# Kernel optimization log

Hardware: AMD Instinct MI355X
Metric: run time of the kernel (lower is better)

Reference implementation:

```python
import jax, jax.numpy as jnp
import numpy as np
import math

B, S, T, F_IN, D = 4, 4096, 4096, 127, 64

def setup_inputs() -> dict:
    key = jax.random.key(0)
    k1, k2, k3, k4 = jax.random.split(key, 4)
    return {
        "x1": jax.random.normal(k1, (B, S, F_IN), dtype=jnp.float32),
        "x2": jax.random.normal(k2, (B, T, F_IN), dtype=jnp.float32),
        "W": jax.random.normal(k3, (D, F_IN), dtype=jnp.float32) * (1.0 / math.sqrt(F_IN)),
        "b": jax.random.normal(k4, (D,), dtype=jnp.float32) * 0.01,
    }

def reference(x1, x2, W, b):
    # shared linear projection: torch Linear -> x @ W.T + b
    q = jnp.einsum('bsf,df->bsd', x1, W) + b   # [B,S,D]
    k = jnp.einsum('btf,df->btd', x2, W) + b   # [B,T,D]
    scores = jnp.einsum('bsd,btd->bst', q, k)  # [B,S,T]
    # faithful to source: v4 = v3.div(1/sqrt(D)) == v3 * sqrt(D)
    scores = scores * jnp.sqrt(jnp.float32(D))
    p = jax.nn.softmax(scores, axis=-1)        # [B,S,T]
    # dropout p=0.01 treated as eval-mode identity (deterministic reference)
    out = jnp.einsum('bst,btf->bsf', p, x2)    # [B,S,F_IN]
    return out
```

## Files before the change

### kernel.cpp

```cpp
#include <hip/hip_runtime.h>
#include <hip/hip_bf16.h>


typedef __bf16 bf16x8 __attribute__((ext_vector_type(8)));
typedef float f32x16 __attribute__((ext_vector_type(16)));

#define S_DIM 4096
#define F_DIM 127
#define QSCALE 11.5415603271f
#define THR 11.0f

static __device__ __forceinline__ unsigned cvt_pk_bf16(float lo, float hi) {
  unsigned r;
  asm("v_cvt_pk_bf16_f32 %0, %1, %2" : "=v"(r) : "v"(lo), "v"(hi));
  return r;
}
static __device__ __forceinline__ float exp2_fast(float x) {
  float r;
  asm("v_exp_f32 %0, %1" : "=v"(r) : "v"(x));
  return r;
}
static __device__ __forceinline__ float m3(float a, float b, float c) {
  return fmaxf(fmaxf(a, b), c);
}
static __device__ __forceinline__ bf16x8 mk_bf16x8(unsigned w0, unsigned w1,
                                                   unsigned w2, unsigned w3) {
  unsigned t[4] = {w0, w1, w2, w3};
  bf16x8 r;
  __builtin_memcpy(&r, t, 16);
  return r;
}
static __device__ __forceinline__ bf16x8 u4_bf16x8(uint4 v) {
  bf16x8 r;
  __builtin_memcpy(&r, &v, 16);
  return r;
}
static __device__ __forceinline__ void split8(float4 a, float4 b, bf16x8& hv,
                                              bf16x8& lv) {
  const unsigned h0 = cvt_pk_bf16(a.x, a.y);
  const unsigned h1 = cvt_pk_bf16(a.z, a.w);
  const unsigned h2 = cvt_pk_bf16(b.x, b.y);
  const unsigned h3 = cvt_pk_bf16(b.z, b.w);
  const unsigned l0 = cvt_pk_bf16(a.x - __uint_as_float(h0 << 16),
                                  a.y - __uint_as_float(h0 & 0xffff0000u));
  const unsigned l1 = cvt_pk_bf16(a.z - __uint_as_float(h1 << 16),
                                  a.w - __uint_as_float(h1 & 0xffff0000u));
  const unsigned l2 = cvt_pk_bf16(b.x - __uint_as_float(h2 << 16),
                                  b.y - __uint_as_float(h2 & 0xffff0000u));
  const unsigned l3 = cvt_pk_bf16(b.z - __uint_as_float(h3 << 16),
                                  b.w - __uint_as_float(h3 & 0xffff0000u));
  hv = mk_bf16x8(h0, h1, h2, h3);
  lv = mk_bf16x8(l0, l1, l2, l3);
}

__global__ __launch_bounds__(256) void prep_kernel(
    const float* __restrict__ x1, const float* __restrict__ x2,
    const float* __restrict__ W, const float* __restrict__ bias,
    uint4* __restrict__ qhf, uint4* __restrict__ qlf,
    uint4* __restrict__ khf, uint4* __restrict__ klf,
    uint4* __restrict__ x2tf) {
  __shared__ unsigned shbuf[8448];
  const int tid = threadIdx.x;
  const int bi = blockIdx.x;

  if (bi >= 256) {
    const int ri = bi - 256;
    const int b = ri >> 8;
    const int tt = ri & 255;
    const int fb = tid >> 6;
    const int l = tid & 63;
    const int t0 = tt * 16 + ((l >> 5) << 3);
    const int f = fb * 32 + (l & 31);
    const float* src = x2 + ((long)b * S_DIM + t0) * F_DIM + f;
    unsigned w[4];
#pragma unroll
    for (int g = 0; g < 4; ++g) {
      const float v0 = (f < F_DIM) ? src[(long)(2 * g) * F_DIM] : 1.0f;
      const float v1 = (f < F_DIM) ? src[(long)(2 * g + 1) * F_DIM] : 1.0f;
      w[g] = cvt_pk_bf16(v0, v1);
    }
    x2tf[((long)(b * 256 + tt) * 4 + fb) * 64 + l] =
        make_uint4(w[0], w[1], w[2], w[3]);
    return;
  }

  float* shw = (float*)shbuf;
  for (int idx = tid; idx < 64 * 128; idx += 256) {
    const int d = idx >> 7;
    const int f = idx & 127;
    shw[d * 132 + f] = (f < F_DIM) ? W[d * F_DIM + f] : 0.f;
  }
  __syncthreads();

  const int wave = tid >> 6;
  const int lane = tid & 63;
  const int arow = lane & 31;
  const int half = lane >> 5;
  const bool isK = bi >= 128;
  const float* x = isK ? x2 : x1;
  const int grow0 = (bi & 127) * 128 + wave * 32;
  const float* xrow = x + (long)(grow0 + arow) * F_DIM;

  bf16x8 xh[8], xl[8];
#pragma unroll
  for (int kk = 0; kk < 8; ++kk) {
    const int f0 = kk * 16 + half * 8;
    float4 a, b;
    a.x = (f0 + 0 < F_DIM) ? xrow[f0 + 0] : 0.f;
    a.y = (f0 + 1 < F_DIM) ? xrow[f0 + 1] : 0.f;
    a.z = (f0 + 2 < F_DIM) ? xrow[f0 + 2] : 0.f;
    a.w = (f0 + 3 < F_DIM) ? xrow[f0 + 3] : 0.f;
    b.x = (f0 + 4 < F_DIM) ? xrow[f0 + 4] : 0.f;
    b.y = (f0 + 5 < F_DIM) ? xrow[f0 + 5] : 0.f;
    b.z = (f0 + 6 < F_DIM) ? xrow[f0 + 6] : 0.f;
    b.w = (f0 + 7 < F_DIM) ? xrow[f0 + 7] : 0.f;
    split8(a, b, xh[kk], xl[kk]);
  }

  f32x16 acc0, acc1;
#pragma unroll
  for (int r = 0; r < 16; ++r) {
    acc0[r] = 0.f;
    acc1[r] = 0.f;
  }
#pragma unroll
  for (int kk = 0; kk < 8; ++kk) {
    const int f0 = kk * 16 + half * 8;
    bf16x8 wh0, wl0, wh1, wl1;
    {
      const float4 a = *(const float4*)&shw[arow * 132 + f0];
      const float4 b = *(const float4*)&shw[arow * 132 + f0 + 4];
      split8(a, b, wh0, wl0);
    }
    {
      const float4 a = *(const float4*)&shw[(32 + arow) * 132 + f0];
      const float4 b = *(const float4*)&shw[(32 + arow) * 132 + f0 + 4];
      split8(a, b, wh1, wl1);
    }
    acc0 = __builtin_amdgcn_mfma_f32_32x32x16_bf16(xh[kk], wh0, acc0, 0, 0, 0);
    acc0 = __builtin_amdgcn_mfma_f32_32x32x16_bf16(xh[kk], wl0, acc0, 0, 0, 0);
    acc0 = __builtin_amdgcn_mfma_f32_32x32x16_bf16(xl[kk], wh0, acc0, 0, 0, 0);
    acc1 = __builtin_amdgcn_mfma_f32_32x32x16_bf16(xh[kk], wh1, acc1, 0, 0, 0);
    acc1 = __builtin_amdgcn_mfma_f32_32x32x16_bf16(xh[kk], wl1, acc1, 0, 0, 0);
    acc1 = __builtin_amdgcn_mfma_f32_32x32x16_bf16(xl[kk], wh1, acc1, 0, 0, 0);
  }
  __syncthreads();

  unsigned* kst = shbuf + wave * 2112;
#pragma unroll
  for (int dt = 0; dt < 2; ++dt) {
    const f32x16 acc = dt ? acc1 : acc0;
    const int d = dt * 32 + arow;
    const float bd = bias[d];
#pragma unroll
    for (int r = 0; r < 16; r += 2) {
      const int row0 = (r & 3) + 8 * (r >> 2) + 4 * half;
      float v0 = acc[r] + bd;
      float v1 = acc[r + 1] + bd;
      if (!isK) {
        v0 *= QSCALE;
        v1 *= QSCALE;
      }
      const unsigned h = cvt_pk_bf16(v0, v1);
      const float l0 = v0 - __uint_as_float(h << 16);
      const float l1 = v1 - __uint_as_float(h & 0xffff0000u);
      const unsigned l = cvt_pk_bf16(l0, l1);
      kst[row0 * 66 + d] = (h & 0xffffu) | (l << 16);
      kst[(row0 + 1) * 66 + d] = (h >> 16) | (l & 0xffff0000u);
    }
  }

  const int b = grow0 >> 12;
  const int tile = (grow0 & (S_DIM - 1)) >> 5;
  uint4* dh = (isK ? khf : qhf) + ((long)(b * 128 + tile) * 4) * 64 + lane;
  uint4* dl = (isK ? klf : qlf) + ((long)(b * 128 + tile) * 4) * 64 + lane;
#pragma unroll
  for (int kk = 0; kk < 4; ++kk) {
    const int d0 = kk * 16 + half * 8;
    unsigned w[8];
#pragma unroll
    for (int j = 0; j < 8; ++j) w[j] = kst[arow * 66 + d0 + j];
    unsigned hw[4], lw[4];
#pragma unroll
    for (int g = 0; g < 4; ++g) {
      hw[g] = (w[2 * g] & 0xffffu) | (w[2 * g + 1] << 16);
      lw[g] = (w[2 * g] >> 16) | (w[2 * g + 1] & 0xffff0000u);
    }
    dh[kk * 64] = make_uint4(hw[0], hw[1], hw[2], hw[3]);
    dl[kk * 64] = make_uint4(lw[0], lw[1], lw[2], lw[3]);
  }
}

__global__ __launch_bounds__(512, 1) void attn_kernel(
    const uint4* __restrict__ qhf, const uint4* __restrict__ qlf,
    const uint4* __restrict__ khf, const uint4* __restrict__ klf,
    const uint4* __restrict__ x2tf, float* __restrict__ out) {
  const int tid = threadIdx.x;
  const int lane = tid & 63;
  const int wave = tid >> 6;
  const int col = lane & 31;
  const int half = lane >> 5;
  const int sub = wave & 1;
  const int qtr = wave >> 1;
  const int bi = blockIdx.x;
  const int xcd = bi & 7;
  const int slot = bi >> 3;
  const int L = (xcd >> 1) * 64 + slot * 2 + (xcd & 1);
  const int b = L >> 6;
  const int q0 = (L & 63) << 6;

  const int qtile = ((q0 + sub * 32) & (S_DIM - 1)) >> 5;
  bf16x8 qh[4], ql[4];
#pragma unroll
  for (int kk = 0; kk < 4; ++kk) {
    qh[kk] = u4_bf16x8(qhf[((long)(b * 128 + qtile) * 4 + kk) * 64 + lane]);
    ql[kk] = u4_bf16x8(qlf[((long)(b * 128 + qtile) * 4 + kk) * 64 + lane]);
  }

  const uint4* khfp = khf + (long)b * 128 * 4 * 64;
  const uint4* klfp = klf + (long)b * 128 * 4 * 64;
  const uint4* xfp = x2tf + (long)b * 256 * 4 * 64;

  f32x16 a0, a1, a2, a3;
#pragma unroll
  for (int r = 0; r < 16; ++r) {
    a0[r] = 0.f; a1[r] = 0.f; a2[r] = 0.f; a3[r] = 0.f;
  }
  float m = -INFINITY;

  uint4 KA[8], KB[8];
#pragma unroll
  for (int kk = 0; kk < 4; ++kk) {
    KA[kk] = khfp[(qtr * 4 + kk) * 64 + lane];
    KA[4 + kk] = klfp[(qtr * 4 + kk) * 64 + lane];
  }

  auto body = [&](const uint4 (&C)[8], uint4 (&N)[8], int i) {
    const int tile = (i << 2) + qtr;
    uint4 xv[8];
#pragma unroll
    for (int kf = 0; kf < 2; ++kf)
#pragma unroll
      for (int fb = 0; fb < 4; ++fb)
        xv[kf * 4 + fb] = xfp[((tile * 2 + kf) * 4 + fb) * 64 + lane];
    if (i < 31) {
      const int tn = ((i + 1) << 2) + qtr;
#pragma unroll
      for (int kk = 0; kk < 4; ++kk) {
        N[kk] = khfp[(tn * 4 + kk) * 64 + lane];
        N[4 + kk] = klfp[(tn * 4 + kk) * 64 + lane];
      }
    }
    f32x16 sa, sb;
#pragma unroll
    for (int r = 0; r < 16; ++r) {
      sa[r] = 0.f;
      sb[r] = 0.f;
    }
    __builtin_amdgcn_s_setprio(1);
#pragma unroll
    for (int kk = 0; kk < 4; ++kk) {
      const bf16x8 kv = u4_bf16x8(C[kk]);
      const bf16x8 lv = u4_bf16x8(C[4 + kk]);
      sa = __builtin_amdgcn_mfma_f32_32x32x16_bf16(kv, qh[kk], sa, 0, 0, 0);
      sb = __builtin_amdgcn_mfma_f32_32x32x16_bf16(kv, ql[kk], sb, 0, 0, 0);
      if (kk < 2)
        sa = __builtin_amdgcn_mfma_f32_32x32x16_bf16(lv, qh[kk], sa, 0, 0, 0);
      else
        sb = __builtin_amdgcn_mfma_f32_32x32x16_bf16(lv, qh[kk], sb, 0, 0, 0);
    }
    __builtin_amdgcn_s_setprio(0);
    f32x16 st;
#pragma unroll
    for (int r = 0; r < 16; ++r) st[r] = sa[r] + sb[r];
    const float e0 = m3(st[0], st[1], st[2]);
    const float e1 = m3(st[3], st[4], st[5]);
    const float e2 = m3(st[6], st[7], st[8]);
    const float e3 = m3(st[9], st[10], st[11]);
    const float e4 = m3(st[12], st[13], st[14]);
    float pmax = fmaxf(m3(e0, e1, e2), m3(e3, e4, st[15]));
    pmax = fmaxf(pmax, __shfl_xor(pmax, 32));
    if (__any(pmax > m + THR)) {
      const float mnew = fmaxf(m, pmax);
      const float sc = exp2_fast(m - mnew);
#pragma unroll
      for (int r = 0; r < 16; ++r) {
        a0[r] *= sc; a1[r] *= sc; a2[r] *= sc; a3[r] *= sc;
      }
      m = mnew;
    }
    unsigned pg[4][2];
#pragma unroll
    for (int g = 0; g < 4; ++g) {
      pg[g][0] = cvt_pk_bf16(exp2_fast(st[4 * g + 0] - m),
                             exp2_fast(st[4 * g + 1] - m));
      pg[g][1] = cvt_pk_bf16(exp2_fast(st[4 * g + 2] - m),
                             exp2_fast(st[4 * g + 3] - m));
    }
    __builtin_amdgcn_s_setprio(1);
#pragma unroll
    for (int kk = 0; kk < 2; ++kk) {
      unsigned x0 = pg[2 * kk][0], y0 = pg[2 * kk + 1][0];
      unsigned x1 = pg[2 * kk][1], y1 = pg[2 * kk + 1][1];
      asm("v_permlane32_swap_b32 %0, %1" : "+v"(x0), "+v"(y0));
      asm("v_permlane32_swap_b32 %0, %1" : "+v"(x1), "+v"(y1));
      const bf16x8 pf = mk_bf16x8(x0, x1, y0, y1);
      a0 = __builtin_amdgcn_mfma_f32_32x32x16_bf16(u4_bf16x8(xv[kk * 4 + 0]),
                                                   pf, a0, 0, 0, 0);
      a1 = __builtin_amdgcn_mfma_f32_32x32x16_bf16(u4_bf16x8(xv[kk * 4 + 1]),
                                                   pf, a1, 0, 0, 0);
      a2 = __builtin_amdgcn_mfma_f32_32x32x16_bf16(u4_bf16x8(xv[kk * 4 + 2]),
                                                   pf, a2, 0, 0, 0);
      a3 = __builtin_amdgcn_mfma_f32_32x32x16_bf16(u4_bf16x8(xv[kk * 4 + 3]),
                                                   pf, a3, 0, 0, 0);
    }
    __builtin_amdgcn_s_setprio(0);
  };

  for (int i = 0; i < 32; i += 2) {
    body(KA, KB, i);
    body(KB, KA, i + 1);
  }

  __shared__ float mbuf[8][32];
  __shared__ float accb[2][128 * 33];
  if (lane < 32) mbuf[wave][col] = m;
  __syncthreads();
  float mstar = mbuf[sub][col];
#pragma unroll
  for (int w = 1; w < 4; ++w) mstar = fmaxf(mstar, mbuf[sub + 2 * w][col]);
  const float wsc = exp2_fast(m - mstar);
  float* buf = accb[sub];
  auto emit = [&](const f32x16& av, int fb, bool first) {
#pragma unroll
    for (int r = 0; r < 16; ++r) {
      const int f = fb * 32 + (r & 3) + 8 * (r >> 2) + 4 * half;
      const float v = av[r] * wsc;
      if (first) buf[f * 33 + col] = v;
      else buf[f * 33 + col] += v;
    }
  };
  for (int p = 0; p < 4; ++p) {
    if (qtr == p) {
      const bool first = (p == 0);
      emit(a0, 0, first);
      emit(a1, 1, first);
      emit(a2, 2, first);
      emit(a3, 3, first);
    }
    __syncthreads();
  }

  const int q64 = tid >> 3;
  const int fg = tid & 7;
  const int s2 = q64 >> 5;
  const int qq = q64 & 31;
  const float inv = 1.0f / accb[s2][127 * 33 + qq];
  float* ob = out + ((long)(b * S_DIM + q0 + q64)) * F_DIM;
#pragma unroll
  for (int j = 0; j < 16; ++j) {
    const int f = fg * 16 + j;
    if (f < F_DIM) ob[f] = accb[s2][f * 33 + qq] * inv;
  }
}

extern "C" void kernel_launch(void* const* d_in, const int* in_sizes, int n_in,
                              void* d_out, int out_size, void* d_ws,
                              size_t ws_size, hipStream_t stream) {
  const float* x1 = (const float*)d_in[0];
  const float* x2 = (const float*)d_in[1];
  const float* W = (const float*)d_in[2];
  const float* bias = (const float*)d_in[3];
  float* out = (float*)d_out;

  char* ws = (char*)d_ws;
  uint4* qhf = (uint4*)ws;
  uint4* qlf = (uint4*)(ws + (2l << 20));
  uint4* khf = (uint4*)(ws + (4l << 20));
  uint4* klf = (uint4*)(ws + (6l << 20));
  uint4* x2tf = (uint4*)(ws + (8l << 20));

  hipLaunchKernelGGL(prep_kernel, dim3(1280), dim3(256), 0, stream, x1, x2, W,
                     bias, qhf, qlf, khf, klf, x2tf);
  hipLaunchKernelGGL(attn_kernel, dim3(256), dim3(512), 0, stream, qhf, qlf,
                     khf, klf, x2tf, out);
}
```

Measured before the change: 87.13 us.

## Stage K and X tiles through shared LDS and skip negligible PV tiles

Each wave pair now splits the global loads: one wave fetches the K hi/lo tile and the other fetches the x2 tile. Both write into a double-buffered 128KB LDS arena that the two waves share through block barriers, so each wave no longer loads its own copies. The three score MFMAs now accumulate into a single register instead of two summed accumulators. The P·V MFMAs are skipped when every score in the tile is more than 26 below the running max, which drops contributions smaller than about 2^-26. The costs are a __syncthreads per iteration, heavier LDS traffic, and a small approximation from the skipped tiles.

Measured after the change: 179.5 us. +106.0%, slower.

```diff
diff --git a/kernel.cpp b/kernel.cpp
--- a/kernel.cpp
+++ b/kernel.cpp
@@ -9,6 +9,7 @@
 #define F_DIM 127
 #define QSCALE 11.5415603271f
 #define THR 11.0f
+#define SKIP 26.0f
 
 static __device__ __forceinline__ unsigned cvt_pk_bf16(float lo, float hi) {
   unsigned r;
@@ -195,6 +196,7 @@
     const uint4* __restrict__ qhf, const uint4* __restrict__ qlf,
     const uint4* __restrict__ khf, const uint4* __restrict__ klf,
     const uint4* __restrict__ x2tf, float* __restrict__ out) {
+  __shared__ __align__(16) char arena[131072];
   const int tid = threadIdx.x;
   const int lane = tid & 63;
   const int wave = tid >> 6;
@@ -221,6 +223,27 @@
   const uint4* klfp = klf + (long)b * 128 * 4 * 64;
   const uint4* xfp = x2tf + (long)b * 256 * 4 * 64;
 
+  char* const myqtr = arena + qtr * 16384;
+
+  auto issue = [&](int t, uint4(&sv)[8]) {
+    if (sub == 0) {
+#pragma unroll
+      for (int kk = 0; kk < 4; ++kk) {
+        sv[kk] = khfp[(t * 4 + kk) * 64 + lane];
+        sv[4 + kk] = klfp[(t * 4 + kk) * 64 + lane];
+      }
+    } else {
+#pragma unroll
+      for (int j = 0; j < 8; ++j)
+        sv[j] = xfp[((t * 2 + (j >> 2)) * 4 + (j & 3)) * 64 + lane];
+    }
+  };
+  auto store = [&](int c, const uint4(&sv)[8]) {
+    char* dst = myqtr + c * 65536 + (sub ? 8192 : 0) + lane * 16;
+#pragma unroll
+    for (int j = 0; j < 8; ++j) *(uint4*)(dst + j * 1024) = sv[j];
+  };
+
   f32x16 a0, a1, a2, a3;
 #pragma unroll
   for (int r = 0; r < 16; ++r) {
@@ -228,51 +251,34 @@
   }
   float m = -INFINITY;
 
-  uint4 KA[8], KB[8];
-#pragma unroll
-  for (int kk = 0; kk < 4; ++kk) {
-    KA[kk] = khfp[(qtr * 4 + kk) * 64 + lane];
-    KA[4 + kk] = klfp[(qtr * 4 + kk) * 64 + lane];
-  }
-
-  auto body = [&](const uint4 (&C)[8], uint4 (&N)[8], int i) {
-    const int tile = (i << 2) + qtr;
-    uint4 xv[8];
-#pragma unroll
-    for (int kf = 0; kf < 2; ++kf)
-#pragma unroll
-      for (int fb = 0; fb < 4; ++fb)
-        xv[kf * 4 + fb] = xfp[((tile * 2 + kf) * 4 + fb) * 64 + lane];
-    if (i < 31) {
-      const int tn = ((i + 1) << 2) + qtr;
-#pragma unroll
-      for (int kk = 0; kk < 4; ++kk) {
-        N[kk] = khfp[(tn * 4 + kk) * 64 + lane];
-        N[4 + kk] = klfp[(tn * 4 + kk) * 64 + lane];
-      }
-    }
-    f32x16 sa, sb;
-#pragma unroll
-    for (int r = 0; r < 16; ++r) {
-      sa[r] = 0.f;
-      sb[r] = 0.f;
-    }
+  {
+    uint4 sv[8];
+    issue(qtr, sv);
+    store(0, sv);
+  }
+  __syncthreads();
+
+  for (int i = 0; i < 32; ++i) {
+    const int c = i & 1;
+    const bool more = (i < 31);
+    uint4 sv[8];
+    if (more) issue(((i + 1) << 2) + qtr, sv);
+
+    const char* src = myqtr + c * 65536 + lane * 16;
+    f32x16 st;
+#pragma unroll
+    for (int r = 0; r < 16; ++r) st[r] = 0.f;
     __builtin_amdgcn_s_setprio(1);
 #pragma unroll
     for (int kk = 0; kk < 4; ++kk) {
-      const bf16x8 kv = u4_bf16x8(C[kk]);
-      const bf16x8 lv = u4_bf16x8(C[4 + kk]);
-      sa = __builtin_amdgcn_mfma_f32_32x32x16_bf16(kv, qh[kk], sa, 0, 0, 0);
-      sb = __builtin_amdgcn_mfma_f32_32x32x16_bf16(kv, ql[kk], sb, 0, 0, 0);
-      if (kk < 2)
-        sa = __builtin_amdgcn_mfma_f32_32x32x16_bf16(lv, qh[kk], sa, 0, 0, 0);
-      else
-        sb = __builtin_amdgcn_mfma_f32_32x32x16_bf16(lv, qh[kk], sb, 0, 0, 0);
+      const bf16x8 kv = *(const bf16x8*)(src + kk * 1024);
+      const bf16x8 lv = *(const bf16x8*)(src + 4096 + kk * 1024);
+      st = __builtin_amdgcn_mfma_f32_32x32x16_bf16(kv, qh[kk], st, 0, 0, 0);
+      st = __builtin_amdgcn_mfma_f32_32x32x16_bf16(kv, ql[kk], st, 0, 0, 0);
+      st = __builtin_amdgcn_mfma_f32_32x32x16_bf16(lv, qh[kk], st, 0, 0, 0);
     }
     __builtin_amdgcn_s_setprio(0);
-    f32x16 st;
-#pragma unroll
-    for (int r = 0; r < 16; ++r) st[r] = sa[r] + sb[r];
+
     const float e0 = m3(st[0], st[1], st[2]);
     const float e1 = m3(st[3], st[4], st[5]);
     const float e2 = m3(st[6], st[7], st[8]);
@@ -289,48 +295,51 @@
       }
       m = mnew;
     }
-    unsigned pg[4][2];
-#pragma unroll
-    for (int g = 0; g < 4; ++g) {
-      pg[g][0] = cvt_pk_bf16(exp2_fast(st[4 * g + 0] - m),
-                             exp2_fast(st[4 * g + 1] - m));
-      pg[g][1] = cvt_pk_bf16(exp2_fast(st[4 * g + 2] - m),
-                             exp2_fast(st[4 * g + 3] - m));
-    }
-    __builtin_amdgcn_s_setprio(1);
-#pragma unroll
-    for (int kk = 0; kk < 2; ++kk) {
-      unsigned x0 = pg[2 * kk][0], y0 = pg[2 * kk + 1][0];
-      unsigned x1 = pg[2 * kk][1], y1 = pg[2 * kk + 1][1];
-      asm("v_permlane32_swap_b32 %0, %1" : "+v"(x0), "+v"(y0));
-      asm("v_permlane32_swap_b32 %0, %1" : "+v"(x1), "+v"(y1));
-      const bf16x8 pf = mk_bf16x8(x0, x1, y0, y1);
-      a0 = __builtin_amdgcn_mfma_f32_32x32x16_bf16(u4_bf16x8(xv[kk * 4 + 0]),
-                                                   pf, a0, 0, 0, 0);
-      a1 = __builtin_amdgcn_mfma_f32_32x32x16_bf16(u4_bf16x8(xv[kk * 4 + 1]),
-                                                   pf, a1, 0, 0, 0);
-      a2 = __builtin_amdgcn_mfma_f32_32x32x16_bf16(u4_bf16x8(xv[kk * 4 + 2]),
-                                                   pf, a2, 0, 0, 0);
-      a3 = __builtin_amdgcn_mfma_f32_32x32x16_bf16(u4_bf16x8(xv[kk * 4 + 3]),
-                                                   pf, a3, 0, 0, 0);
-    }
-    __builtin_amdgcn_s_setprio(0);
-  };
-
-  for (int i = 0; i < 32; i += 2) {
-    body(KA, KB, i);
-    body(KB, KA, i + 1);
-  }
-
-  __shared__ float mbuf[8][32];
-  __shared__ float accb[2][128 * 33];
-  if (lane < 32) mbuf[wave][col] = m;
+    if (__any(pmax > m - SKIP)) {
+      uint4 xv[8];
+#pragma unroll
+      for (int j = 0; j < 8; ++j)
+        xv[j] = *(const uint4*)(src + 8192 + j * 1024);
+      unsigned pg[4][2];
+#pragma unroll
+      for (int g = 0; g < 4; ++g) {
+        pg[g][0] = cvt_pk_bf16(exp2_fast(st[4 * g + 0] - m),
+                               exp2_fast(st[4 * g + 1] - m));
+        pg[g][1] = cvt_pk_bf16(exp2_fast(st[4 * g + 2] - m),
+                               exp2_fast(st[4 * g + 3] - m));
+      }
+      __builtin_amdgcn_s_setprio(1);
+#pragma unroll
+      for (int kk = 0; kk < 2; ++kk) {
+        unsigned x0 = pg[2 * kk][0], y0 = pg[2 * kk + 1][0];
+        unsigned x1 = pg[2 * kk][1], y1 = pg[2 * kk + 1][1];
+        asm("v_permlane32_swap_b32 %0, %1" : "+v"(x0), "+v"(y0));
+        asm("v_permlane32_swap_b32 %0, %1" : "+v"(x1), "+v"(y1));
+        const bf16x8 pf = mk_bf16x8(x0, x1, y0, y1);
+        a0 = __builtin_amdgcn_mfma_f32_32x32x16_bf16(u4_bf16x8(xv[kk * 4 + 0]),
+                                                     pf, a0, 0, 0, 0);
+        a1 = __builtin_amdgcn_mfma_f32_32x32x16_bf16(u4_bf16x8(xv[kk * 4 + 1]),
+                                                     pf, a1, 0, 0, 0);
+        a2 = __builtin_amdgcn_mfma_f32_32x32x16_bf16(u4_bf16x8(xv[kk * 4 + 2]),
+                                                     pf, a2, 0, 0, 0);
+        a3 = __builtin_amdgcn_mfma_f32_32x32x16_bf16(u4_bf16x8(xv[kk * 4 + 3]),
+                                                     pf, a3, 0, 0, 0);
+      }
+      __builtin_amdgcn_s_setprio(0);
+    }
+    if (more) store(c ^ 1, sv);
+    __syncthreads();
+  }
+
+  float* accb = (float*)arena;
+  float* mb = (float*)(arena + 33792);
+  if (lane < 32) mb[wave * 32 + col] = m;
   __syncthreads();
-  float mstar = mbuf[sub][col];
-#pragma unroll
-  for (int w = 1; w < 4; ++w) mstar = fmaxf(mstar, mbuf[sub + 2 * w][col]);
+  float mstar = mb[sub * 32 + col];
+#pragma unroll
+  for (int w = 1; w < 4; ++w) mstar = fmaxf(mstar, mb[(sub + 2 * w) * 32 + col]);
   const float wsc = exp2_fast(m - mstar);
-  float* buf = accb[sub];
+  float* buf = accb + sub * (128 * 33);
   auto emit = [&](const f32x16& av, int fb, bool first) {
 #pragma unroll
     for (int r = 0; r < 16; ++r) {
@@ -355,12 +364,12 @@
   const int fg = tid & 7;
   const int s2 = q64 >> 5;
   const int qq = q64 & 31;
-  const float inv = 1.0f / accb[s2][127 * 33 + qq];
+  const float inv = 1.0f / accb[s2 * (128 * 33) + 127 * 33 + qq];
   float* ob = out + ((long)(b * S_DIM + q0 + q64)) * F_DIM;
 #pragma unroll
   for (int j = 0; j < 16; ++j) {
     const int f = fg * 16 + j;
-    if (f < F_DIM) ob[f] = accb[s2][f * 33 + qq] * inv;
+    if (f < F_DIM) ob[f] = accb[s2 * (128 * 33) + f * 33 + qq] * inv;
   }
 }
 
```

## Skip negligible PV tiles and split attention into smaller 256-thread blocks

Applied to the files above, without the earlier changes.

Adds a per-tile check that skips loading x2 and the probability-times-value MFMAs when all scores in the tile are more than 26 (log2 units) below the running max, since their exponentials underflow bf16 relevance. Also restructures the grid to 512 blocks of 4 waves each handling 32 queries, with two blocks per CU, simplifying the cross-wave reduction. The skip trades exactness for work reduction and its benefit depends on how peaked the softmax is; smaller blocks reduce K reuse per block.

Measured after the change: 78.25 us. 1.11x faster.

```diff
diff --git a/kernel.cpp b/kernel.cpp
--- a/kernel.cpp
+++ b/kernel.cpp
@@ -9,6 +9,7 @@
 #define F_DIM 127
 #define QSCALE 11.5415603271f
 #define THR 11.0f
+#define SKIP 26.0f
 
 static __device__ __forceinline__ unsigned cvt_pk_bf16(float lo, float hi) {
   unsigned r;
@@ -191,7 +192,7 @@
   }
 }
 
-__global__ __launch_bounds__(512, 1) void attn_kernel(
+__global__ __launch_bounds__(256, 2) void attn_kernel(
     const uint4* __restrict__ qhf, const uint4* __restrict__ qlf,
     const uint4* __restrict__ khf, const uint4* __restrict__ klf,
     const uint4* __restrict__ x2tf, float* __restrict__ out) {
@@ -200,21 +201,17 @@
   const int wave = tid >> 6;
   const int col = lane & 31;
   const int half = lane >> 5;
-  const int sub = wave & 1;
-  const int qtr = wave >> 1;
   const int bi = blockIdx.x;
-  const int xcd = bi & 7;
-  const int slot = bi >> 3;
-  const int L = (xcd >> 1) * 64 + slot * 2 + (xcd & 1);
-  const int b = L >> 6;
-  const int q0 = (L & 63) << 6;
-
-  const int qtile = ((q0 + sub * 32) & (S_DIM - 1)) >> 5;
+  const int L = (bi & 7) * 64 + (bi >> 3);
+  const int b = L >> 7;
+  const int qt = L & 127;
+  const int q0 = qt << 5;
+
   bf16x8 qh[4], ql[4];
 #pragma unroll
   for (int kk = 0; kk < 4; ++kk) {
-    qh[kk] = u4_bf16x8(qhf[((long)(b * 128 + qtile) * 4 + kk) * 64 + lane]);
-    ql[kk] = u4_bf16x8(qlf[((long)(b * 128 + qtile) * 4 + kk) * 64 + lane]);
+    qh[kk] = u4_bf16x8(qhf[((long)(b * 128 + qt) * 4 + kk) * 64 + lane]);
+    ql[kk] = u4_bf16x8(qlf[((long)(b * 128 + qt) * 4 + kk) * 64 + lane]);
   }
 
   const uint4* khfp = khf + (long)b * 128 * 4 * 64;
@@ -231,20 +228,14 @@
   uint4 KA[8], KB[8];
 #pragma unroll
   for (int kk = 0; kk < 4; ++kk) {
-    KA[kk] = khfp[(qtr * 4 + kk) * 64 + lane];
-    KA[4 + kk] = klfp[(qtr * 4 + kk) * 64 + lane];
+    KA[kk] = khfp[(wave * 4 + kk) * 64 + lane];
+    KA[4 + kk] = klfp[(wave * 4 + kk) * 64 + lane];
   }
 
   auto body = [&](const uint4 (&C)[8], uint4 (&N)[8], int i) {
-    const int tile = (i << 2) + qtr;
-    uint4 xv[8];
-#pragma unroll
-    for (int kf = 0; kf < 2; ++kf)
-#pragma unroll
-      for (int fb = 0; fb < 4; ++fb)
-        xv[kf * 4 + fb] = xfp[((tile * 2 + kf) * 4 + fb) * 64 + lane];
+    const int tile = (i << 2) + wave;
     if (i < 31) {
-      const int tn = ((i + 1) << 2) + qtr;
+      const int tn = ((i + 1) << 2) + wave;
 #pragma unroll
       for (int kk = 0; kk < 4; ++kk) {
         N[kk] = khfp[(tn * 4 + kk) * 64 + lane];
@@ -270,15 +261,14 @@
         sb = __builtin_amdgcn_mfma_f32_32x32x16_bf16(lv, qh[kk], sb, 0, 0, 0);
     }
     __builtin_amdgcn_s_setprio(0);
-    f32x16 st;
-#pragma unroll
-    for (int r = 0; r < 16; ++r) st[r] = sa[r] + sb[r];
-    const float e0 = m3(st[0], st[1], st[2]);
-    const float e1 = m3(st[3], st[4], st[5]);
-    const float e2 = m3(st[6], st[7], st[8]);
-    const float e3 = m3(st[9], st[10], st[11]);
-    const float e4 = m3(st[12], st[13], st[14]);
-    float pmax = fmaxf(m3(e0, e1, e2), m3(e3, e4, st[15]));
+#pragma unroll
+    for (int r = 0; r < 16; ++r) sa[r] += sb[r];
+    const float e0 = m3(sa[0], sa[1], sa[2]);
+    const float e1 = m3(sa[3], sa[4], sa[5]);
+    const float e2 = m3(sa[6], sa[7], sa[8]);
+    const float e3 = m3(sa[9], sa[10], sa[11]);
+    const float e4 = m3(sa[12], sa[13], sa[14]);
+    float pmax = fmaxf(m3(e0, e1, e2), m3(e3, e4, sa[15]));
     pmax = fmaxf(pmax, __shfl_xor(pmax, 32));
     if (__any(pmax > m + THR)) {
       const float mnew = fmaxf(m, pmax);
@@ -289,32 +279,38 @@
       }
       m = mnew;
     }
-    unsigned pg[4][2];
-#pragma unroll
-    for (int g = 0; g < 4; ++g) {
-      pg[g][0] = cvt_pk_bf16(exp2_fast(st[4 * g + 0] - m),
-                             exp2_fast(st[4 * g + 1] - m));
-      pg[g][1] = cvt_pk_bf16(exp2_fast(st[4 * g + 2] - m),
-                             exp2_fast(st[4 * g + 3] - m));
-    }
-    __builtin_amdgcn_s_setprio(1);
-#pragma unroll
-    for (int kk = 0; kk < 2; ++kk) {
-      unsigned x0 = pg[2 * kk][0], y0 = pg[2 * kk + 1][0];
-      unsigned x1 = pg[2 * kk][1], y1 = pg[2 * kk + 1][1];
-      asm("v_permlane32_swap_b32 %0, %1" : "+v"(x0), "+v"(y0));
-      asm("v_permlane32_swap_b32 %0, %1" : "+v"(x1), "+v"(y1));
-      const bf16x8 pf = mk_bf16x8(x0, x1, y0, y1);
-      a0 = __builtin_amdgcn_mfma_f32_32x32x16_bf16(u4_bf16x8(xv[kk * 4 + 0]),
-                                                   pf, a0, 0, 0, 0);
-      a1 = __builtin_amdgcn_mfma_f32_32x32x16_bf16(u4_bf16x8(xv[kk * 4 + 1]),
-                                                   pf, a1, 0, 0, 0);
-      a2 = __builtin_amdgcn_mfma_f32_32x32x16_bf16(u4_bf16x8(xv[kk * 4 + 2]),
-                                                   pf, a2, 0, 0, 0);
-      a3 = __builtin_amdgcn_mfma_f32_32x32x16_bf16(u4_bf16x8(xv[kk * 4 + 3]),
-                                                   pf, a3, 0, 0, 0);
-    }
-    __builtin_amdgcn_s_setprio(0);
+    if (__any(pmax > m - SKIP)) {
+      uint4 xv[8];
+#pragma unroll
+      for (int j = 0; j < 8; ++j)
+        xv[j] = xfp[((tile * 2 + (j >> 2)) * 4 + (j & 3)) * 64 + lane];
+      unsigned pg[4][2];
+#pragma unroll
+      for (int g = 0; g < 4; ++g) {
+        pg[g][0] = cvt_pk_bf16(exp2_fast(sa[4 * g + 0] - m),
+                               exp2_fast(sa[4 * g + 1] - m));
+        pg[g][1] = cvt_pk_bf16(exp2_fast(sa[4 * g + 2] - m),
+                               exp2_fast(sa[4 * g + 3] - m));
+      }
+      __builtin_amdgcn_s_setprio(1);
+#pragma unroll
+      for (int kk = 0; kk < 2; ++kk) {
+        unsigned x0 = pg[2 * kk][0], y0 = pg[2 * kk + 1][0];
+        unsigned x1 = pg[2 * kk][1], y1 = pg[2 * kk + 1][1];
+        asm("v_permlane32_swap_b32 %0, %1" : "+v"(x0), "+v"(y0));
+        asm("v_permlane32_swap_b32 %0, %1" : "+v"(x1), "+v"(y1));
+        const bf16x8 pf = mk_bf16x8(x0, x1, y0, y1);
+        a0 = __builtin_amdgcn_mfma_f32_32x32x16_bf16(u4_bf16x8(xv[kk * 4 + 0]),
+                                                     pf, a0, 0, 0, 0);
+        a1 = __builtin_amdgcn_mfma_f32_32x32x16_bf16(u4_bf16x8(xv[kk * 4 + 1]),
+                                                     pf, a1, 0, 0, 0);
+        a2 = __builtin_amdgcn_mfma_f32_32x32x16_bf16(u4_bf16x8(xv[kk * 4 + 2]),
+                                                     pf, a2, 0, 0, 0);
+        a3 = __builtin_amdgcn_mfma_f32_32x32x16_bf16(u4_bf16x8(xv[kk * 4 + 3]),
+                                                     pf, a3, 0, 0, 0);
+      }
+      __builtin_amdgcn_s_setprio(0);
+    }
   };
 
   for (int i = 0; i < 32; i += 2) {
@@ -322,26 +318,24 @@
     body(KB, KA, i + 1);
   }
 
-  __shared__ float mbuf[8][32];
-  __shared__ float accb[2][128 * 33];
+  __shared__ float mbuf[4][32];
+  __shared__ float accbuf[128 * 33];
   if (lane < 32) mbuf[wave][col] = m;
   __syncthreads();
-  float mstar = mbuf[sub][col];
-#pragma unroll
-  for (int w = 1; w < 4; ++w) mstar = fmaxf(mstar, mbuf[sub + 2 * w][col]);
+  const float mstar = fmaxf(fmaxf(mbuf[0][col], mbuf[1][col]),
+                            fmaxf(mbuf[2][col], mbuf[3][col]));
   const float wsc = exp2_fast(m - mstar);
-  float* buf = accb[sub];
   auto emit = [&](const f32x16& av, int fb, bool first) {
 #pragma unroll
     for (int r = 0; r < 16; ++r) {
       const int f = fb * 32 + (r & 3) + 8 * (r >> 2) + 4 * half;
       const float v = av[r] * wsc;
-      if (first) buf[f * 33 + col] = v;
-      else buf[f * 33 + col] += v;
+      if (first) accbuf[f * 33 + col] = v;
+      else accbuf[f * 33 + col] += v;
     }
   };
   for (int p = 0; p < 4; ++p) {
-    if (qtr == p) {
+    if (wave == p) {
       const bool first = (p == 0);
       emit(a0, 0, first);
       emit(a1, 1, first);
@@ -351,16 +345,14 @@
     __syncthreads();
   }
 
-  const int q64 = tid >> 3;
+  const int q = tid >> 3;
   const int fg = tid & 7;
-  const int s2 = q64 >> 5;
-  const int qq = q64 & 31;
-  const float inv = 1.0f / accb[s2][127 * 33 + qq];
-  float* ob = out + ((long)(b * S_DIM + q0 + q64)) * F_DIM;
+  const float inv = 1.0f / accbuf[127 * 33 + q];
+  float* ob = out + ((long)(b * S_DIM + q0 + q)) * F_DIM;
 #pragma unroll
   for (int j = 0; j < 16; ++j) {
     const int f = fg * 16 + j;
-    if (f < F_DIM) ob[f] = accb[s2][f * 33 + qq] * inv;
+    if (f < F_DIM) ob[f] = accbuf[f * 33 + q] * inv;
   }
 }
 
@@ -382,6 +374,6 @@
 
   hipLaunchKernelGGL(prep_kernel, dim3(1280), dim3(256), 0, stream, x1, x2, W,
                      bias, qhf, qlf, khf, klf, x2tf);
-  hipLaunchKernelGGL(attn_kernel, dim3(256), dim3(512), 0, stream, qhf, qlf,
+  hipLaunchKernelGGL(attn_kernel, dim3(512), dim3(256), 0, stream, qhf, qlf,
                      khf, klf, x2tf, out);
 }
```
